# Kernel tuning notes

Hardware: AMD Instinct MI355X
Metric: run time of the kernel (lower is better)

Reference implementation:

```python
import jax, jax.numpy as jnp
import numpy as np

G = 8            # group_order
KS = 3           # kernel size
C1, O1 = 1, 16   # gconv1 channels
C2, O2 = 16, 32  # gconv2 channels
HW = 28
NUM_CLASSES = 10


def _bilinear_sample(img, px, py):
    # img: (O, I, K, K); px, py: (K, K) pixel coords; zero padding outside
    # (matches torch grid_sample bilinear, align_corners=False, padding_mode='zeros')
    K = img.shape[-1]
    x0 = jnp.floor(px); y0 = jnp.floor(py)
    wx = px - x0; wy = py - y0
    x0i = x0.astype(jnp.int32); y0i = y0.astype(jnp.int32)

    def gather(yi, xi):
        valid = (yi >= 0) & (yi < K) & (xi >= 0) & (xi < K)
        yc = jnp.clip(yi, 0, K - 1)
        xc = jnp.clip(xi, 0, K - 1)
        return img[:, :, yc, xc] * valid.astype(img.dtype)  # (O,I,K,K)

    return (gather(y0i, x0i) * (1 - wx) * (1 - wy)
            + gather(y0i, x0i + 1) * wx * (1 - wy)
            + gather(y0i + 1, x0i) * (1 - wx) * wy
            + gather(y0i + 1, x0i + 1) * wx * wy)


def _rotated_kernels(base, group_order):
    # Replicates F.affine_grid + F.grid_sample (align_corners=False) for each rotation k.
    K = base.shape[-1]
    coords = (2.0 * jnp.arange(K, dtype=base.dtype) + 1.0) / K - 1.0  # normalized centers
    xs, ys = jnp.meshgrid(coords, coords, indexing='xy')  # x along width, y along height

    def rot_k(k):
        theta = 2.0 * np.pi * k / group_order
        c, s = jnp.cos(theta), jnp.sin(theta)
        gx = c * xs - s * ys   # theta row [cos, -sin, 0]
        gy = s * xs + c * ys   # theta row [sin,  cos, 0]
        px = ((gx + 1.0) * K - 1.0) / 2.0  # unnormalize, align_corners=False
        py = ((gy + 1.0) * K - 1.0) / 2.0
        return _bilinear_sample(base, px, py)

    return jax.vmap(rot_k)(jnp.arange(group_order, dtype=base.dtype))  # (G,O,I,K,K)


def _conv2d(x, w, pad):
    return jax.lax.conv_general_dilated(
        x, w, window_strides=(1, 1), padding=[(pad, pad), (pad, pad)],
        dimension_numbers=('NCHW', 'OIHW', 'NCHW'))


def setup_inputs() -> dict:
    key = jax.random.key(0)
    k1, k2, k3, k4, k5 = jax.random.split(key, 5)
    x = jax.random.normal(k1, (512, C1, HW, HW), dtype=jnp.float32)
    base_weight = jax.random.normal(k2, (O1, C1, KS, KS), dtype=jnp.float32)
    w2 = jax.random.normal(k3, (O2, C2, G, KS, KS), dtype=jnp.float32) * 0.05
    fc_w = jax.random.normal(k4, (NUM_CLASSES, O2 * HW * HW), dtype=jnp.float32) * 0.01
    fc_b = jax.random.normal(k5, (NUM_CLASSES,), dtype=jnp.float32) * 0.01
    return {"x": x, "base_weight": base_weight, "w2": w2, "fc_w": fc_w, "fc_b": fc_b}


def reference(x, base_weight, w2, fc_w, fc_b):
    B = x.shape[0]
    # --- GroupConv2D: steerable rotated kernels, concat along out-channels (k-major) ---
    rk = _rotated_kernels(base_weight, G)           # (G, O1, C1, K, K)
    w1 = rk.reshape(G * O1, C1, KS, KS)
    h = _conv2d(x, w1, 1)                           # (B, G*O1, 28, 28)
    h = jax.nn.relu(h)                              # GroupReLU == plain ReLU

    # --- GroupToGroupConv: circulant structure fused into one conv ---
    # torch: out channel = g*O2 + o (cat dim=1), in channel = c*G + h_idx (view layout)
    g = jnp.arange(G)[:, None]
    hh = jnp.arange(G)[None, :]
    idx = (g - hh) % G                               # (G, G)
    Wc = w2[:, :, idx]                               # (O2, C2, G_g, G_h, K, K)
    Wbig = jnp.transpose(Wc, (2, 0, 1, 3, 4, 5)).reshape(G * O2, C2 * G, KS, KS)
    h2 = _conv2d(h, Wbig, 1)                         # (B, G*O2, 28, 28)
    h2 = jax.nn.relu(h2)

    # --- GroupPooling (mean over the *inner* factor of 8, as in the torch view) ---
    p = h2.reshape(B, (G * O2) // G, G, HW, HW).mean(axis=2)  # (B, 32, 28, 28)

    # --- fc ---
    flat = p.reshape(B, -1)
    return flat @ fc_w.T + fc_b
```

## Files before the change

kernel.cpp:

```cpp
#include <hip/hip_runtime.h>
#include <hip/hip_bf16.h>
#include <cstdint>

#define AS1 __attribute__((address_space(1)))
#define AS3 __attribute__((address_space(3)))

typedef __bf16 bf16x8 __attribute__((ext_vector_type(8)));
typedef float  f32x16 __attribute__((ext_vector_type(16)));

__device__ __forceinline__ void gld_lds16(const void* g, void* l) {
    __builtin_amdgcn_global_load_lds((const AS1 void*)g, (AS3 void*)l, 16, 0, 0);
}

__global__ __launch_bounds__(256) void k_rot(const float* __restrict__ base,
                                             const float* __restrict__ w2,
                                             float* __restrict__ w1,
                                             __hip_bfloat16* __restrict__ A) {
    int tid = threadIdx.x;
    if (blockIdx.x == 0) {
        if (tid < 128) {
            int m = tid;
            int g = m >> 4, o = m & 15;
            float th = 6.28318530717958647692f * (float)g / 8.0f;
            float c = cosf(th), s = sinf(th);
            for (int i = 0; i < 3; ++i) {
                float ys = (2.0f * i + 1.0f) / 3.0f - 1.0f;
                for (int j = 0; j < 3; ++j) {
                    float xs = (2.0f * j + 1.0f) / 3.0f - 1.0f;
                    float gx = c * xs - s * ys;
                    float gy = s * xs + c * ys;
                    float px = ((gx + 1.0f) * 3.0f - 1.0f) * 0.5f;
                    float py = ((gy + 1.0f) * 3.0f - 1.0f) * 0.5f;
                    float x0 = floorf(px), y0 = floorf(py);
                    float wx = px - x0, wy = py - y0;
                    int x0i = (int)x0, y0i = (int)y0;
                    auto gat = [&](int yi, int xi) -> float {
                        bool v = (yi >= 0) && (yi < 3) && (xi >= 0) && (xi < 3);
                        int yc = min(max(yi, 0), 2), xc = min(max(xi, 0), 2);
                        return v ? base[o * 9 + yc * 3 + xc] : 0.0f;
                    };
                    w1[m * 9 + i * 3 + j] =
                          gat(y0i, x0i)         * (1.0f - wx) * (1.0f - wy)
                        + gat(y0i, x0i + 1)     * wx          * (1.0f - wy)
                        + gat(y0i + 1, x0i)     * (1.0f - wx) * wy
                        + gat(y0i + 1, x0i + 1) * wx          * wy;
                }
            }
        }
    } else {
        int i = (blockIdx.x - 1) * 256 + tid;
        int r = i / 1152, k = i - r * 1152;
        int g = r >> 5, o2 = r & 31;
        int kk = k >> 7, cch = k & 127;
        int ky = kk / 3, kx = kk - ky * 3;
        int c2 = cch >> 3, hh = cch & 7;
        int gi = (g - hh) & 7;
        float val = w2[((o2 * 16 + c2) * 8 + gi) * 9 + ky * 3 + kx];
        int half = cch >> 6, kt = cch & 63;
        int t = kk * 2 + half, ks2 = kt >> 4, hi2 = (kt >> 3) & 1, e = kt & 7;
        int mh = r >> 7, i2 = (r >> 5) & 3, row = r & 31;
        int aidx = ((((t * 2 + mh) * 16) + i2 * 4 + ks2) << 9) + ((hi2 << 5) + row) * 8 + e;
        A[aidx] = __float2bfloat16(val);
    }
}

__global__ __launch_bounds__(256) void k_conv1(const float* __restrict__ x,
                                               const float* __restrict__ w1g,
                                               __hip_bfloat16* __restrict__ hl) {
    int tid = threadIdx.x;

    __shared__ float w1s[1152];
    for (int i = tid; i < 1152; i += 256) w1s[i] = w1g[i];
    __syncthreads();

    const int c0 = (tid & 15) * 8;
    float wreg[8][9];
#pragma unroll
    for (int cc = 0; cc < 8; ++cc)
#pragma unroll
        for (int k = 0; k < 9; ++k) wreg[cc][k] = w1s[(c0 + cc) * 9 + k];

    const int slot = tid >> 4;
    const int band = blockIdx.x % 15;
    const int b    = blockIdx.x / 15;
    const int yy   = band * 2 + (slot >> 3);
    const int xx0  = (slot & 7) * 4;

    const float* xb = x + b * 784;
    float xv[3][6];
#pragma unroll
    for (int t = 0; t < 3; ++t) {
        int sy = yy - 2 + t;
        bool syok = (sy >= 0) && (sy < 28);
#pragma unroll
        for (int u = 0; u < 6; ++u) {
            int sx = xx0 - 2 + u;
            bool ok = syok && (sx >= 0) && (sx < 28);
            xv[t][u] = ok ? xb[sy * 28 + sx] : 0.0f;
        }
    }

    float acc[4][8];
#pragma unroll
    for (int j = 0; j < 4; ++j)
#pragma unroll
        for (int cc = 0; cc < 8; ++cc) acc[j][cc] = 0.0f;

#pragma unroll
    for (int t = 0; t < 3; ++t)
#pragma unroll
        for (int u = 0; u < 3; ++u) {
#pragma unroll
            for (int j = 0; j < 4; ++j) {
                float xvv = xv[t][j + u];
#pragma unroll
                for (int cc = 0; cc < 8; ++cc)
                    acc[j][cc] += xvv * wreg[cc][t * 3 + u];
            }
        }

#pragma unroll
    for (int j = 0; j < 4; ++j) {
        int xx = xx0 + j;
        if (xx < 30) {
            bool interior = (yy >= 1) && (yy <= 28) && (xx >= 1) && (xx <= 28);
            union { __hip_bfloat16 h[8]; float4 f4; } u;
#pragma unroll
            for (int cc = 0; cc < 8; ++cc)
                u.h[cc] = __float2bfloat16(interior ? fmaxf(acc[j][cc], 0.0f) : 0.0f);
            int pi = b * 900 + yy * 30 + xx;
            *(float4*)(hl + (size_t)pi * 128 + c0) = u.f4;
        }
    }
}

__global__ __launch_bounds__(512, 2) void k_conv2(const __hip_bfloat16* __restrict__ A,
                                                  const __hip_bfloat16* __restrict__ hl,
                                                  __hip_bfloat16* __restrict__ p) {
    __shared__ __align__(16) char smem[131072];

    const int tid  = threadIdx.x;
    const int lane = tid & 63;
    const int w    = tid >> 6;
    const int hi   = lane >> 5;
    const int wqr  = w >> 2;
    const int wqc  = w & 3;

    const int bid = blockIdx.x;
    const int nt  = (bid & 7) * 196 + (bid >> 3);
    const int n0  = nt << 8;

    uint32_t bSrc[2][2], ldsCh[2];
#pragma unroll
    for (int q = 0; q < 2; ++q) {
        int ch = 2 * w + q;
        int rl = ch * 8 + (lane >> 3);
        int ca = (lane & 7) ^ (rl & 7) ^ (ch & 3);
        ldsCh[q] = (uint32_t)(ch * 1024);
#pragma unroll
        for (int hn = 0; hn < 2; ++hn) {
            int n = n0 + hn * 128 + rl;
            int b = n / 784; int rr = n - b * 784;
            int y = rr / 28; int xx = rr - y * 28;
            bSrc[q][hn] = (uint32_t)(((b * 30 + y) * 30 + xx) * 256 + ca * 16);
        }
    }

    uint32_t bRd[2]; int bSw[2];
#pragma unroll
    for (int j = 0; j < 2; ++j) {
        int r = wqc * 64 + j * 32 + (lane & 31);
        bRd[j] = (uint32_t)((r >> 7) * 16384 + (r & 127) * 128);
        bSw[j] = (r & 7) ^ ((r >> 3) & 3);
    }

    const uint32_t aRd = (uint32_t)(wqr * 16384 + lane * 16);

    f32x16 acc[4][2];
#pragma unroll
    for (int i = 0; i < 4; ++i)
#pragma unroll
        for (int j = 0; j < 2; ++j) acc[i][j] = (f32x16)(0.0f);

    const char* Ab = (const char*)A;
    const char* Hb = (const char*)hl;

    auto stage = [&](int tt, char* dst) {
#pragma unroll
        for (int q = 0; q < 4; ++q)
            gld_lds16(Ab + (size_t)tt * 32768 + q * 8192 + tid * 16,
                      dst + q * 8192 + tid * 16);
        int kk = tt >> 1, half = tt & 1;
        int ky = kk / 3, kx = kk - ky * 3;
        uint32_t boff = (uint32_t)((ky * 30 + kx) * 256 + half * 128);
        gld_lds16(Hb + bSrc[0][0] + boff, dst + 32768 + ldsCh[0]);
        gld_lds16(Hb + bSrc[1][0] + boff, dst + 32768 + ldsCh[1]);
        gld_lds16(Hb + bSrc[0][1] + boff, dst + 49152 + ldsCh[0]);
        gld_lds16(Hb + bSrc[1][1] + boff, dst + 49152 + ldsCh[1]);
    };

    stage(0, smem);

#pragma unroll 1
    for (int t = 0; t < 17; ++t) {
        __syncthreads();
        char* cur = smem + ((t & 1) << 16);
        const char* LA = cur + aRd;
        const char* LB = cur + 32768;
        stage(t + 1, smem + (((t + 1) & 1) << 16));

        bf16x8 aF[2][4], bF[2][2];
#pragma unroll
        for (int i = 0; i < 4; ++i)
            aF[0][i] = *(const bf16x8*)(LA + ((i * 4 + 0) << 10));
#pragma unroll
        for (int j = 0; j < 2; ++j)
            bF[0][j] = *(const bf16x8*)(LB + bRd[j] + ((uint32_t)((0 + hi) ^ bSw[j]) << 4));

#pragma unroll
        for (int ks = 0; ks < 4; ++ks) {
            const int c = ks & 1, nx = c ^ 1;
            if (ks < 3) {
#pragma unroll
                for (int i = 0; i < 4; ++i)
                    aF[nx][i] = *(const bf16x8*)(LA + ((i * 4 + ks + 1) << 10));
#pragma unroll
                for (int j = 0; j < 2; ++j)
                    bF[nx][j] = *(const bf16x8*)(LB + bRd[j] + ((uint32_t)(((ks + 1) * 2 + hi) ^ bSw[j]) << 4));
            }
#pragma unroll
            for (int i = 0; i < 4; ++i)
#pragma unroll
                for (int j = 0; j < 2; ++j)
                    acc[i][j] = __builtin_amdgcn_mfma_f32_32x32x16_bf16(aF[c][i], bF[c][j], acc[i][j], 0, 0, 0);
        }

        __builtin_amdgcn_sched_group_barrier(0x030, 8, 0);
        __builtin_amdgcn_sched_group_barrier(0x100, 6, 0);
#pragma unroll
        for (int ks = 0; ks < 3; ++ks) {
#pragma unroll
            for (int r = 0; r < 6; ++r) {
                __builtin_amdgcn_sched_group_barrier(0x008, 1, 0);
                __builtin_amdgcn_sched_group_barrier(0x100, 1, 0);
            }
            __builtin_amdgcn_sched_group_barrier(0x008, 2, 0);
        }
        __builtin_amdgcn_sched_group_barrier(0x008, 8, 0);
    }

    {
        __syncthreads();
        char* cur = smem + 65536;
        const char* LA = cur + aRd;
        const char* LB = cur + 32768;

        bf16x8 aF[2][4], bF[2][2];
#pragma unroll
        for (int i = 0; i < 4; ++i)
            aF[0][i] = *(const bf16x8*)(LA + ((i * 4 + 0) << 10));
#pragma unroll
        for (int j = 0; j < 2; ++j)
            bF[0][j] = *(const bf16x8*)(LB + bRd[j] + ((uint32_t)((0 + hi) ^ bSw[j]) << 4));

#pragma unroll
        for (int ks = 0; ks < 4; ++ks) {
            const int c = ks & 1, nx = c ^ 1;
            if (ks < 3) {
#pragma unroll
                for (int i = 0; i < 4; ++i)
                    aF[nx][i] = *(const bf16x8*)(LA + ((i * 4 + ks + 1) << 10));
#pragma unroll
                for (int j = 0; j < 2; ++j)
                    bF[nx][j] = *(const bf16x8*)(LB + bRd[j] + ((uint32_t)(((ks + 1) * 2 + hi) ^ bSw[j]) << 4));
            }
#pragma unroll
            for (int i = 0; i < 4; ++i)
#pragma unroll
                for (int j = 0; j < 2; ++j)
                    acc[i][j] = __builtin_amdgcn_mfma_f32_32x32x16_bf16(aF[c][i], bF[c][j], acc[i][j], 0, 0, 0);
        }
    }

#pragma unroll
    for (int i = 0; i < 4; ++i) {
#pragma unroll
        for (int j = 0; j < 2; ++j) {
            f32x16 v = acc[i][j];
#pragma unroll
            for (int u = 0; u < 4; ++u) {
                float sv = fmaxf(v[4*u], 0.0f) + fmaxf(v[4*u+1], 0.0f)
                         + fmaxf(v[4*u+2], 0.0f) + fmaxf(v[4*u+3], 0.0f);
                sv += __shfl_xor(sv, 32, 64);
                if (hi == 0) {
                    int a = wqr * 16 + i * 4 + u;
                    int n = n0 + wqc * 64 + j * 32 + (lane & 31);
                    int b = n / 784; int rr = n - b * 784;
                    p[(b * 32 + a) * 784 + rr] = __float2bfloat16(sv * 0.125f);
                }
            }
        }
    }
}

__global__ __launch_bounds__(256) void k_fc(const __hip_bfloat16* __restrict__ p,
                                            const float* __restrict__ fw,
                                            const float* __restrict__ fb,
                                            float* __restrict__ out) {
    int b = blockIdx.x >> 2, ks = blockIdx.x & 3;
    int tid = threadIdx.x;
    const bf16x8* pb = (const bf16x8*)(p + (size_t)b * 25088);
    const float4* w4 = (const float4*)fw;
    float acc[10] = {};
    for (int t = ks * 784 + tid; t < (ks + 1) * 784; t += 256) {
        union { bf16x8 v; __hip_bfloat16 h[8]; } u;
        u.v = pb[t];
        float vf[8];
#pragma unroll
        for (int e = 0; e < 8; ++e) vf[e] = __bfloat162float(u.h[e]);
#pragma unroll
        for (int c = 0; c < 10; ++c) {
            float4 u0 = w4[c * 6272 + 2 * t];
            float4 u1 = w4[c * 6272 + 2 * t + 1];
            acc[c] += vf[0] * u0.x + vf[1] * u0.y + vf[2] * u0.z + vf[3] * u0.w
                    + vf[4] * u1.x + vf[5] * u1.y + vf[6] * u1.z + vf[7] * u1.w;
        }
    }
    __shared__ float red[10][4];
    int lane = tid & 63, wv = tid >> 6;
#pragma unroll
    for (int c = 0; c < 10; ++c) {
        float s = acc[c];
#pragma unroll
        for (int o = 32; o > 0; o >>= 1) s += __shfl_down(s, o, 64);
        if (lane == 0) red[c][wv] = s;
    }
    __syncthreads();
    if (tid < 10) {
        float s = red[tid][0] + red[tid][1] + red[tid][2] + red[tid][3];
        if (ks == 0) s += fb[tid];
        atomicAdd(&out[b * 10 + tid], s);
    }
}

extern "C" void kernel_launch(void* const* d_in, const int* in_sizes, int n_in,
                              void* d_out, int out_size, void* d_ws, size_t ws_size,
                              hipStream_t stream) {
    const float* x  = (const float*)d_in[0];
    const float* bw = (const float*)d_in[1];
    const float* w2 = (const float*)d_in[2];
    const float* fw = (const float*)d_in[3];
    const float* fb = (const float*)d_in[4];
    float* out = (float*)d_out;
    char* ws = (char*)d_ws;

    float*          w1   = (float*)(ws);
    __hip_bfloat16* Amat = (__hip_bfloat16*)(ws + 4608);
    __hip_bfloat16* hl   = (__hip_bfloat16*)(ws + 594432);
    __hip_bfloat16* p    = (__hip_bfloat16*)(ws + 118563328);

    hipMemsetAsync(d_out, 0, (size_t)out_size * sizeof(float), stream);
    k_rot  <<<1153, 256, 0, stream>>>(bw, w2, w1, Amat);
    k_conv1<<<7680, 256, 0, stream>>>(x, w1, hl);
    k_conv2<<<1568, 512, 0, stream>>>(Amat, hl, p);
    k_fc   <<<2048, 256, 0, stream>>>(p, fw, fb, out);
}
```

Before: 345.6 us.

## Batch eight samples per fc block to reuse loaded weight vectors

The fc kernel now processes eight batch rows per block and loads each fc weight slice once into registers, reusing it across all eight rows. This cuts redundant weight reads from global/L2 by a factor of eight, and the grid shrinks to 256 blocks. In exchange, each thread holds 80 accumulators plus 20 float4 weights, raising register pressure and lowering occupancy and parallelism.

```diff
diff --git a/kernel.cpp b/kernel.cpp
--- a/kernel.cpp
+++ b/kernel.cpp
@@ -307,39 +307,53 @@
                                             const float* __restrict__ fw,
                                             const float* __restrict__ fb,
                                             float* __restrict__ out) {
-    int b = blockIdx.x >> 2, ks = blockIdx.x & 3;
+    int bg = blockIdx.x >> 2, ks = blockIdx.x & 3;
     int tid = threadIdx.x;
-    const bf16x8* pb = (const bf16x8*)(p + (size_t)b * 25088);
     const float4* w4 = (const float4*)fw;
-    float acc[10] = {};
+    float acc[8][10];
+#pragma unroll
+    for (int bb = 0; bb < 8; ++bb)
+#pragma unroll
+        for (int c = 0; c < 10; ++c) acc[bb][c] = 0.0f;
+
     for (int t = ks * 784 + tid; t < (ks + 1) * 784; t += 256) {
-        union { bf16x8 v; __hip_bfloat16 h[8]; } u;
-        u.v = pb[t];
-        float vf[8];
-#pragma unroll
-        for (int e = 0; e < 8; ++e) vf[e] = __bfloat162float(u.h[e]);
+        float4 u0[10], u1[10];
 #pragma unroll
         for (int c = 0; c < 10; ++c) {
-            float4 u0 = w4[c * 6272 + 2 * t];
-            float4 u1 = w4[c * 6272 + 2 * t + 1];
-            acc[c] += vf[0] * u0.x + vf[1] * u0.y + vf[2] * u0.z + vf[3] * u0.w
-                    + vf[4] * u1.x + vf[5] * u1.y + vf[6] * u1.z + vf[7] * u1.w;
-        }
-    }
-    __shared__ float red[10][4];
+            u0[c] = w4[c * 6272 + 2 * t];
+            u1[c] = w4[c * 6272 + 2 * t + 1];
+        }
+#pragma unroll
+        for (int bb = 0; bb < 8; ++bb) {
+            union { bf16x8 v; __hip_bfloat16 h[8]; } u;
+            u.v = *(const bf16x8*)(p + (size_t)(bg * 8 + bb) * 25088 + (size_t)t * 8);
+            float vf[8];
+#pragma unroll
+            for (int e = 0; e < 8; ++e) vf[e] = __bfloat162float(u.h[e]);
+#pragma unroll
+            for (int c = 0; c < 10; ++c)
+                acc[bb][c] += vf[0] * u0[c].x + vf[1] * u0[c].y + vf[2] * u0[c].z + vf[3] * u0[c].w
+                            + vf[4] * u1[c].x + vf[5] * u1[c].y + vf[6] * u1[c].z + vf[7] * u1[c].w;
+        }
+    }
+
+    __shared__ float red[8][10][4];
     int lane = tid & 63, wv = tid >> 6;
 #pragma unroll
-    for (int c = 0; c < 10; ++c) {
-        float s = acc[c];
-#pragma unroll
-        for (int o = 32; o > 0; o >>= 1) s += __shfl_down(s, o, 64);
-        if (lane == 0) red[c][wv] = s;
-    }
+    for (int bb = 0; bb < 8; ++bb)
+#pragma unroll
+        for (int c = 0; c < 10; ++c) {
+            float s = acc[bb][c];
+#pragma unroll
+            for (int o = 32; o > 0; o >>= 1) s += __shfl_down(s, o, 64);
+            if (lane == 0) red[bb][c][wv] = s;
+        }
     __syncthreads();
-    if (tid < 10) {
-        float s = red[tid][0] + red[tid][1] + red[tid][2] + red[tid][3];
-        if (ks == 0) s += fb[tid];
-        atomicAdd(&out[b * 10 + tid], s);
+    if (tid < 80) {
+        int bb = tid / 10, c = tid - bb * 10;
+        float s = red[bb][c][0] + red[bb][c][1] + red[bb][c][2] + red[bb][c][3];
+        if (ks == 0) s += fb[c];
+        atomicAdd(&out[(bg * 8 + bb) * 10 + c], s);
     }
 }
 
@@ -363,5 +377,5 @@
     k_rot  <<<1153, 256, 0, stream>>>(bw, w2, w1, Amat);
     k_conv1<<<7680, 256, 0, stream>>>(x, w1, hl);
     k_conv2<<<1568, 512, 0, stream>>>(Amat, hl, p);
-    k_fc   <<<2048, 256, 0, stream>>>(p, fw, fb, out);
-}
+    k_fc   <<<256,  256, 0, stream>>>(p, fw, fb, out);
+}
```

After: 333.6 us. 3.5% less time.
